# Performance work log

Measured on AMD Instinct MI355X. Metric: run time of the kernel, lower is better.

The kernel has to match this reference:

```python
import jax, jax.numpy as jnp
import numpy as np

R = 2.0            # distance exponent
Q = 1.0            # activation exponent
SPECIFICITY = 1.0  # c in exp(-c * dist)
BETA = 3.0         # lateral competition exponent
TEMP_COMP = 1.0    # ClusterCompetition temperature
TEMP_WTA = 0.1     # SoftWTA temperature
PHI = 1.5          # association scaling
NEG_INF = -1e30

B, C, D = 1024, 512, 256


def setup_inputs() -> dict:
    key = jax.random.key(0)
    k1, k2, k3, k4, k5 = jax.random.split(key, 5)
    inp = jax.random.normal(k1, (B, D), dtype=jnp.float32)
    w_dist = jax.random.normal(k2, (C, D), dtype=jnp.float32)      # cluster centers
    attn = jax.random.uniform(k3, (D,), dtype=jnp.float32)         # dim-wise attention (>=0)
    w_assoc = jax.random.normal(k4, (C, 2), dtype=jnp.float32)     # association weights
    mask = jax.random.randint(k5, (C,), 0, 2, dtype=jnp.int32)     # recruited-cluster mask
    return {"inp": inp, "w_dist": w_dist, "attn": attn, "w_assoc": w_assoc, "mask": mask}


def reference(inp, w_dist, attn, w_assoc, mask):
    m = mask.astype(inp.dtype)                       # [C] 0/1 recruited gate
    # Distance: per-dim |x - w|^r for every (item, cluster) pair -> [B, C, D]
    dim_dist = jnp.abs(inp[:, None, :] - w_dist[None, :, :]) ** R
    # DimWiseAttention: sum-to-one constrained attention over dims
    a = attn / jnp.sum(attn)
    # ClusterActivation: H_j = exp(-c * (sum_d a_d * dist_d)^(q/r)) -> [B, C]
    wdist = jnp.einsum('bcd,d->bc', dim_dist, a)
    H = jnp.exp(-SPECIFICITY * wdist ** (Q / R))
    clusters_actv = H * m                            # MaskNonRecruit
    nonzero = m > 0
    # ClusterCompetition: softmax over recruited clusters of actv^beta (temp-scaled),
    # re-weighting each cluster's own activation.
    comp_logits = jnp.where(nonzero, BETA * jnp.log(H) / TEMP_COMP, NEG_INF)
    p_comp = jax.nn.softmax(comp_logits, axis=-1)
    competed = p_comp * clusters_actv                # [B, C]
    # SoftWTA: plain temperature softmax over recruited clusters, same re-weighting.
    wta_logits = jnp.where(nonzero, competed / TEMP_WTA, NEG_INF)
    p_wta = jax.nn.softmax(wta_logits, axis=-1)
    softwta = p_wta * competed                       # [B, C]
    # Classification: Phi-scaled linear readout to 2 classes.
    y_pred = PHI * (softwta @ w_assoc)               # [B, 2]
    return y_pred
```

## Files before the change

### kernel.cpp

```cpp
#include <hip/hip_runtime.h>
#include <math.h>

#define BN 1024
#define CN 512
#define DN 256
#define ROWS 4
#define WAVES 8
#define KC (DN / WAVES)

#define XS_OFF 0
#define R_OFF  (BN * DN)
#define Q_OFF  (R_OFF + BN)

__launch_bounds__(256, 4)
__global__ void prep_kernel(const float* __restrict__ inp, const float* __restrict__ wd,
                            const float* __restrict__ attn, float* __restrict__ ws) {
    __shared__ float red[4];
    float* xs = ws + XS_OFF;
    float* r  = ws + R_OFF;
    float* q  = ws + Q_OFF;

    const int tid  = threadIdx.x;
    const int lane = tid & 63;
    const int blk  = blockIdx.x;

    float av = attn[tid];
    float s = av;
    #pragma unroll
    for (int off = 32; off > 0; off >>= 1) s += __shfl_xor(s, off);
    if (lane == 0) red[tid >> 6] = s;
    __syncthreads();
    const float a = av / (red[0] + red[1] + red[2] + red[3]);

    float c;
    if (blk < BN) {
        const float x = inp[blk * DN + tid];
        xs[blk * DN + tid] = a * x;
        c = a * x * x;
    } else {
        const float w = wd[(blk - BN) * DN + tid];
        c = a * w * w;
    }
    #pragma unroll
    for (int off = 32; off > 0; off >>= 1) c += __shfl_xor(c, off);
    __syncthreads();
    if (lane == 0) red[tid >> 6] = c;
    __syncthreads();
    if (tid == 0) {
        const float tot = red[0] + red[1] + red[2] + red[3];
        if (blk < BN) r[blk] = tot; else q[blk - BN] = tot;
    }
}

#define NEG_INF_F (-1e30f)

__device__ __forceinline__ float waveMax(float v) {
    #pragma unroll
    for (int off = 32; off > 0; off >>= 1) v = fmaxf(v, __shfl_xor(v, off));
    return v;
}
__device__ __forceinline__ float waveSum(float v) {
    #pragma unroll
    for (int off = 32; off > 0; off >>= 1) v += __shfl_xor(v, off);
    return v;
}

__launch_bounds__(512, 1)
__global__ void fused_kernel(const float* __restrict__ ws, const float* __restrict__ wd,
                             const int* __restrict__ mask, const float* __restrict__ w_assoc,
                             float* __restrict__ y) {
    __shared__ float red[WAVES * 32 * 64];

    const int tid  = threadIdx.x;
    const int lane = tid & 63;
    const int wz   = __builtin_amdgcn_readfirstlane(tid >> 6);
    const int b0   = blockIdx.x * ROWS;
    const int kbase = wz * KC;

    const float* xs = ws + XS_OFF;

    const float* wp[8];
    #pragma unroll
    for (int j = 0; j < 8; ++j)
        wp[j] = wd + (size_t)(lane + 64 * j) * DN + kbase;

    float acc[ROWS][8] = {};

    #pragma unroll
    for (int k4 = 0; k4 < KC / 4; ++k4) {
        float4 xv[ROWS];
        #pragma unroll
        for (int rr = 0; rr < ROWS; ++rr) {
            const int idx = __builtin_amdgcn_readfirstlane((b0 + rr) * DN + kbase + 4 * k4);
            xv[rr] = *(const float4*)&xs[idx];
        }
        #pragma unroll
        for (int j = 0; j < 8; ++j) {
            const float4 w4 = *(const float4*)(wp[j] + 4 * k4);
            #pragma unroll
            for (int rr = 0; rr < ROWS; ++rr) {
                float t = fmaf(xv[rr].x, w4.x, acc[rr][j]);
                t = fmaf(xv[rr].y, w4.y, t);
                t = fmaf(xv[rr].z, w4.z, t);
                acc[rr][j] = fmaf(xv[rr].w, w4.w, t);
            }
        }
    }

    #pragma unroll
    for (int rr = 0; rr < ROWS; ++rr)
        #pragma unroll
        for (int j = 0; j < 8; ++j)
            red[(wz * 32 + rr * 8 + j) * 64 + lane] = acc[rr][j];
    __syncthreads();

    if (wz < ROWS) {
        const int rr = wz;

        float dot[8] = {};
        #pragma unroll
        for (int z = 0; z < WAVES; ++z)
            #pragma unroll
            for (int j = 0; j < 8; ++j)
                dot[j] += red[(z * 32 + rr * 8 + j) * 64 + lane];

        const float rb = ws[R_OFF + b0 + rr];

        float t[8]; bool rec[8];
        #pragma unroll
        for (int j = 0; j < 8; ++j) {
            const int c = lane + 64 * j;
            const float wdist = fmaxf(rb + ws[Q_OFF + c] - 2.0f * dot[j], 0.0f);
            t[j] = sqrtf(wdist);
            rec[j] = mask[c] > 0;
        }

        float l1[8], lmax = NEG_INF_F;
        #pragma unroll
        for (int j = 0; j < 8; ++j) { l1[j] = rec[j] ? (-3.0f * t[j]) : NEG_INF_F; lmax = fmaxf(lmax, l1[j]); }
        const float mx1 = waveMax(lmax);
        float e1[8], lsum = 0.f;
        #pragma unroll
        for (int j = 0; j < 8; ++j) { e1[j] = rec[j] ? expf(l1[j] - mx1) : 0.f; lsum += e1[j]; }
        const float inv_s1 = 1.0f / waveSum(lsum);

        float competed[8];
        #pragma unroll
        for (int j = 0; j < 8; ++j) competed[j] = e1[j] * inv_s1 * expf(-t[j]);

        float l2[8]; lmax = NEG_INF_F;
        #pragma unroll
        for (int j = 0; j < 8; ++j) { l2[j] = rec[j] ? (competed[j] * 10.0f) : NEG_INF_F; lmax = fmaxf(lmax, l2[j]); }
        const float mx2 = waveMax(lmax);
        float e2[8]; lsum = 0.f;
        #pragma unroll
        for (int j = 0; j < 8; ++j) { e2[j] = rec[j] ? expf(l2[j] - mx2) : 0.f; lsum += e2[j]; }
        const float inv_s2 = 1.0f / waveSum(lsum);

        float y0 = 0.f, y1 = 0.f;
        #pragma unroll
        for (int j = 0; j < 8; ++j) {
            const int c = lane + 64 * j;
            const float sw = e2[j] * inv_s2 * competed[j];
            const float2 wa = *(const float2*)&w_assoc[2 * c];
            y0 = fmaf(sw, wa.x, y0);
            y1 = fmaf(sw, wa.y, y1);
        }
        y0 = waveSum(y0);
        y1 = waveSum(y1);
        if (lane == 0) {
            float2 o = {1.5f * y0, 1.5f * y1};
            *(float2*)&y[(b0 + rr) * 2] = o;
        }
    }
}

extern "C" void kernel_launch(void* const* d_in, const int* in_sizes, int n_in,
                              void* d_out, int out_size, void* d_ws, size_t ws_size,
                              hipStream_t stream) {
    const float* inp     = (const float*)d_in[0];
    const float* w_dist  = (const float*)d_in[1];
    const float* attn    = (const float*)d_in[2];
    const float* w_assoc = (const float*)d_in[3];
    const int*   mask    = (const int*)d_in[4];
    float* out = (float*)d_out;
    float* ws  = (float*)d_ws;

    prep_kernel<<<BN + CN, 256, 0, stream>>>(inp, w_dist, attn, ws);
    fused_kernel<<<BN / ROWS, 512, 0, stream>>>(ws, w_dist, mask, w_assoc, out);
}
```

Measured before the change: 87.83 us.

## Transpose sqrt-attention-scaled centers and compute direct squared differences

The prep kernel now scales both inputs and cluster centers by sqrt(attention) and writes a transposed [D, C] copy of the centers through an LDS tile. This lets the main kernel read contiguous float4 center values per lane and accumulate (x-w)^2 directly, instead of using the norm-expansion dot product. Prep launches far fewer blocks, and the mask and association weights are read with vectorized loads, with cluster indices remapped to 4*lane+k. The direct difference adds a subtract per FMA, so the main loop does more arithmetic, and the transpose adds extra workspace traffic in prep.

After: 74.70 us. 1.18x faster.

```diff
diff --git a/kernel.cpp b/kernel.cpp
--- a/kernel.cpp
+++ b/kernel.cpp
@@ -5,104 +5,120 @@
 #define CN 512
 #define DN 256
 #define ROWS 4
-#define WAVES 8
-#define KC (DN / WAVES)
+#define DW 32
 
 #define XS_OFF 0
-#define R_OFF  (BN * DN)
-#define Q_OFF  (R_OFF + BN)
+#define WT_OFF (BN * DN)
+
+#define NEG_INF_F (-1e30f)
+
+__device__ __forceinline__ float waveMax(float v) {
+    #pragma unroll
+    for (int off = 32; off > 0; off >>= 1) v = fmaxf(v, __shfl_xor(v, off));
+    return v;
+}
+__device__ __forceinline__ float waveSum(float v) {
+    #pragma unroll
+    for (int off = 32; off > 0; off >>= 1) v += __shfl_xor(v, off);
+    return v;
+}
 
 __launch_bounds__(256, 4)
 __global__ void prep_kernel(const float* __restrict__ inp, const float* __restrict__ wd,
                             const float* __restrict__ attn, float* __restrict__ ws) {
-    __shared__ float red[4];
-    float* xs = ws + XS_OFF;
-    float* r  = ws + R_OFF;
-    float* q  = ws + Q_OFF;
+    __shared__ float red4[4];
+    __shared__ float sarr[DN];
+    __shared__ __align__(16) float tile[64][65];
 
     const int tid  = threadIdx.x;
     const int lane = tid & 63;
-    const int blk  = blockIdx.x;
 
     float av = attn[tid];
     float s = av;
     #pragma unroll
     for (int off = 32; off > 0; off >>= 1) s += __shfl_xor(s, off);
-    if (lane == 0) red[tid >> 6] = s;
+    if (lane == 0) red4[tid >> 6] = s;
     __syncthreads();
-    const float a = av / (red[0] + red[1] + red[2] + red[3]);
-
-    float c;
-    if (blk < BN) {
-        const float x = inp[blk * DN + tid];
-        xs[blk * DN + tid] = a * x;
-        c = a * x * x;
+    const float sv = sqrtf(av / (red4[0] + red4[1] + red4[2] + red4[3]));
+    sarr[tid] = sv;
+    __syncthreads();
+
+    const int blk = blockIdx.x;
+    if (blk < BN / 4) {
+        #pragma unroll
+        for (int i = 0; i < 4; ++i) {
+            const int r = blk * 4 + i;
+            ws[XS_OFF + r * DN + tid] = inp[r * DN + tid] * sv;
+        }
     } else {
-        const float w = wd[(blk - BN) * DN + tid];
-        c = a * w * w;
+        const int tb = blk - BN / 4;
+        const int c0 = (tb & 7) * 64;
+        const int d0 = (tb >> 3) * 64;
+        const int cr = tid >> 2;
+        const int q  = tid & 3;
+        #pragma unroll
+        for (int i = 0; i < 4; ++i) {
+            const int dd = q * 16 + i * 4;
+            float4 w4 = *(const float4*)&wd[(c0 + cr) * DN + d0 + dd];
+            w4.x *= sarr[d0 + dd + 0]; w4.y *= sarr[d0 + dd + 1];
+            w4.z *= sarr[d0 + dd + 2]; w4.w *= sarr[d0 + dd + 3];
+            *(float4*)&tile[cr][dd] = w4;
+        }
+        __syncthreads();
+        const int dr = tid >> 2;
+        #pragma unroll
+        for (int i = 0; i < 4; ++i) {
+            const int cc = q * 16 + i * 4;
+            float4 o = {tile[cc + 0][dr], tile[cc + 1][dr],
+                        tile[cc + 2][dr], tile[cc + 3][dr]};
+            *(float4*)&ws[WT_OFF + (d0 + dr) * CN + c0 + cc] = o;
+        }
     }
-    #pragma unroll
-    for (int off = 32; off > 0; off >>= 1) c += __shfl_xor(c, off);
-    __syncthreads();
-    if (lane == 0) red[tid >> 6] = c;
-    __syncthreads();
-    if (tid == 0) {
-        const float tot = red[0] + red[1] + red[2] + red[3];
-        if (blk < BN) r[blk] = tot; else q[blk - BN] = tot;
-    }
-}
-
-#define NEG_INF_F (-1e30f)
-
-__device__ __forceinline__ float waveMax(float v) {
-    #pragma unroll
-    for (int off = 32; off > 0; off >>= 1) v = fmaxf(v, __shfl_xor(v, off));
-    return v;
-}
-__device__ __forceinline__ float waveSum(float v) {
-    #pragma unroll
-    for (int off = 32; off > 0; off >>= 1) v += __shfl_xor(v, off);
-    return v;
 }
 
 __launch_bounds__(512, 1)
-__global__ void fused_kernel(const float* __restrict__ ws, const float* __restrict__ wd,
-                             const int* __restrict__ mask, const float* __restrict__ w_assoc,
-                             float* __restrict__ y) {
-    __shared__ float red[WAVES * 32 * 64];
+__global__ void dist_kernel(const float* __restrict__ ws, const int* __restrict__ mask,
+                            const float* __restrict__ w_assoc, float* __restrict__ y) {
+    __shared__ float comb[8 * 32 * 64];
 
     const int tid  = threadIdx.x;
     const int lane = tid & 63;
     const int wz   = __builtin_amdgcn_readfirstlane(tid >> 6);
     const int b0   = blockIdx.x * ROWS;
-    const int kbase = wz * KC;
 
     const float* xs = ws + XS_OFF;
-
-    const float* wp[8];
-    #pragma unroll
-    for (int j = 0; j < 8; ++j)
-        wp[j] = wd + (size_t)(lane + 64 * j) * DN + kbase;
+    const float* wT = ws + WT_OFF;
+    const int d0w = wz * DW;
 
     float acc[ROWS][8] = {};
 
     #pragma unroll
-    for (int k4 = 0; k4 < KC / 4; ++k4) {
+    for (int ch = 0; ch < DW / 4; ++ch) {
+        const int d0 = d0w + ch * 4;
         float4 xv[ROWS];
         #pragma unroll
         for (int rr = 0; rr < ROWS; ++rr) {
-            const int idx = __builtin_amdgcn_readfirstlane((b0 + rr) * DN + kbase + 4 * k4);
+            const int idx = __builtin_amdgcn_readfirstlane((b0 + rr) * DN + d0);
             xv[rr] = *(const float4*)&xs[idx];
         }
         #pragma unroll
-        for (int j = 0; j < 8; ++j) {
-            const float4 w4 = *(const float4*)(wp[j] + 4 * k4);
+        for (int dd = 0; dd < 4; ++dd) {
+            const float* wrow = &wT[(size_t)(d0 + dd) * CN];
+            const float4 wa = *(const float4*)&wrow[4 * lane];
+            const float4 wb = *(const float4*)&wrow[256 + 4 * lane];
             #pragma unroll
             for (int rr = 0; rr < ROWS; ++rr) {
-                float t = fmaf(xv[rr].x, w4.x, acc[rr][j]);
-                t = fmaf(xv[rr].y, w4.y, t);
-                t = fmaf(xv[rr].z, w4.z, t);
-                acc[rr][j] = fmaf(xv[rr].w, w4.w, t);
+                const float xu = (dd == 0) ? xv[rr].x : (dd == 1) ? xv[rr].y
+                               : (dd == 2) ? xv[rr].z : xv[rr].w;
+                float e;
+                e = xu - wa.x; acc[rr][0] = fmaf(e, e, acc[rr][0]);
+                e = xu - wa.y; acc[rr][1] = fmaf(e, e, acc[rr][1]);
+                e = xu - wa.z; acc[rr][2] = fmaf(e, e, acc[rr][2]);
+                e = xu - wa.w; acc[rr][3] = fmaf(e, e, acc[rr][3]);
+                e = xu - wb.x; acc[rr][4] = fmaf(e, e, acc[rr][4]);
+                e = xu - wb.y; acc[rr][5] = fmaf(e, e, acc[rr][5]);
+                e = xu - wb.z; acc[rr][6] = fmaf(e, e, acc[rr][6]);
+                e = xu - wb.w; acc[rr][7] = fmaf(e, e, acc[rr][7]);
             }
         }
     }
@@ -111,29 +127,25 @@
     for (int rr = 0; rr < ROWS; ++rr)
         #pragma unroll
         for (int j = 0; j < 8; ++j)
-            red[(wz * 32 + rr * 8 + j) * 64 + lane] = acc[rr][j];
+            comb[(wz * 32 + rr * 8 + j) * 64 + lane] = acc[rr][j];
     __syncthreads();
 
     if (wz < ROWS) {
         const int rr = wz;
-
-        float dot[8] = {};
-        #pragma unroll
-        for (int z = 0; z < WAVES; ++z)
+        float dist[8] = {};
+        #pragma unroll
+        for (int zz = 0; zz < 8; ++zz)
             #pragma unroll
             for (int j = 0; j < 8; ++j)
-                dot[j] += red[(z * 32 + rr * 8 + j) * 64 + lane];
-
-        const float rb = ws[R_OFF + b0 + rr];
+                dist[j] += comb[(zz * 32 + rr * 8 + j) * 64 + lane];
 
         float t[8]; bool rec[8];
-        #pragma unroll
-        for (int j = 0; j < 8; ++j) {
-            const int c = lane + 64 * j;
-            const float wdist = fmaxf(rb + ws[Q_OFF + c] - 2.0f * dot[j], 0.0f);
-            t[j] = sqrtf(wdist);
-            rec[j] = mask[c] > 0;
-        }
+        const int4 m0 = *(const int4*)&mask[4 * lane];
+        const int4 m1 = *(const int4*)&mask[256 + 4 * lane];
+        rec[0] = m0.x > 0; rec[1] = m0.y > 0; rec[2] = m0.z > 0; rec[3] = m0.w > 0;
+        rec[4] = m1.x > 0; rec[5] = m1.y > 0; rec[6] = m1.z > 0; rec[7] = m1.w > 0;
+        #pragma unroll
+        for (int j = 0; j < 8; ++j) t[j] = sqrtf(dist[j]);
 
         float l1[8], lmax = NEG_INF_F;
         #pragma unroll
@@ -157,15 +169,22 @@
         for (int j = 0; j < 8; ++j) { e2[j] = rec[j] ? expf(l2[j] - mx2) : 0.f; lsum += e2[j]; }
         const float inv_s2 = 1.0f / waveSum(lsum);
 
+        const float4 waA = *(const float4*)&w_assoc[8 * lane];
+        const float4 waB = *(const float4*)&w_assoc[8 * lane + 4];
+        const float4 waC = *(const float4*)&w_assoc[512 + 8 * lane];
+        const float4 waD = *(const float4*)&w_assoc[512 + 8 * lane + 4];
+        float sw[8];
+        #pragma unroll
+        for (int j = 0; j < 8; ++j) sw[j] = e2[j] * inv_s2 * competed[j];
         float y0 = 0.f, y1 = 0.f;
-        #pragma unroll
-        for (int j = 0; j < 8; ++j) {
-            const int c = lane + 64 * j;
-            const float sw = e2[j] * inv_s2 * competed[j];
-            const float2 wa = *(const float2*)&w_assoc[2 * c];
-            y0 = fmaf(sw, wa.x, y0);
-            y1 = fmaf(sw, wa.y, y1);
-        }
+        y0 = fmaf(sw[0], waA.x, y0); y1 = fmaf(sw[0], waA.y, y1);
+        y0 = fmaf(sw[1], waA.z, y0); y1 = fmaf(sw[1], waA.w, y1);
+        y0 = fmaf(sw[2], waB.x, y0); y1 = fmaf(sw[2], waB.y, y1);
+        y0 = fmaf(sw[3], waB.z, y0); y1 = fmaf(sw[3], waB.w, y1);
+        y0 = fmaf(sw[4], waC.x, y0); y1 = fmaf(sw[4], waC.y, y1);
+        y0 = fmaf(sw[5], waC.z, y0); y1 = fmaf(sw[5], waC.w, y1);
+        y0 = fmaf(sw[6], waD.x, y0); y1 = fmaf(sw[6], waD.y, y1);
+        y0 = fmaf(sw[7], waD.z, y0); y1 = fmaf(sw[7], waD.w, y1);
         y0 = waveSum(y0);
         y1 = waveSum(y1);
         if (lane == 0) {
@@ -186,6 +205,6 @@
     float* out = (float*)d_out;
     float* ws  = (float*)d_ws;
 
-    prep_kernel<<<BN + CN, 256, 0, stream>>>(inp, w_dist, attn, ws);
-    fused_kernel<<<BN / ROWS, 512, 0, stream>>>(ws, w_dist, mask, w_assoc, out);
-}
+    prep_kernel<<<BN / 4 + 32, 256, 0, stream>>>(inp, w_dist, attn, ws);
+    dist_kernel<<<BN / ROWS, 512, 0, stream>>>(ws, mask, w_assoc, out);
+}
```
